# Kernel tuning notes

Measured on AMD Instinct MI355X. Metric: run time of the kernel, lower is better.

Reference implementation:

```python
import jax, jax.numpy as jnp
import numpy as np

NA, NF, EA, EF, NG = 200000, 50000, 800000, 200000, 4096
D = 128
BN_EPS = 1e-5

def _bn(x, g, b):
    m = x.mean(axis=0)
    v = x.var(axis=0)
    return g * (x - m) * jax.lax.rsqrt(v + BN_EPS) + b

def _gine(x, src, dst, edge_emb, W1, b1, g1, be1, W2, b2):
    # message = relu(x_src + edge_emb); scatter-add to dst; (1+eps)*x with eps=0
    msg = jax.nn.relu(x[src] + edge_emb)
    agg = jax.ops.segment_sum(msg, dst, num_segments=x.shape[0])
    h = x + agg
    h = jax.nn.relu(_bn(h @ W1 + b1, g1, be1))
    return h @ W2 + b2

def _seg_mean(x, idx, n):
    s = jax.ops.segment_sum(x, idx, num_segments=n)
    c = jax.ops.segment_sum(jnp.ones((x.shape[0],), x.dtype), idx, num_segments=n)
    return s / jnp.maximum(c, 1.0)[:, None]

def setup_inputs() -> dict:
    key = jax.random.key(0)
    ks = jax.random.split(key, 40)
    def nrm(i, shape, scale=0.05):
        return (jax.random.normal(ks[i], shape, dtype=jnp.float32) * scale)
    inp = {
        'atom_x': jax.random.normal(ks[0], (NA, 101), dtype=jnp.float32),
        'fg_x': jax.random.normal(ks[1], (NF, 73), dtype=jnp.float32),
        'atom_edge_attr': jax.random.normal(ks[2], (EA, 11), dtype=jnp.float32),
        'fg_edge_attr': jax.random.normal(ks[3], (EF, 101), dtype=jnp.float32),
        'atom_emb_W': nrm(4, (101, D)), 'atom_emb_b': jnp.zeros((D,), jnp.float32),
        'fg_emb_W': nrm(5, (73, D)), 'fg_emb_b': jnp.zeros((D,), jnp.float32),
        'bond_W': nrm(6, (3, 11, D)), 'bond_b': jnp.zeros((3, D), jnp.float32),
        'ag_W1': nrm(7, (3, D, 2 * D)), 'ag_b1': jnp.zeros((3, 2 * D), jnp.float32),
        'ag_g1': jnp.ones((3, 2 * D), jnp.float32), 'ag_be1': jnp.zeros((3, 2 * D), jnp.float32),
        'ag_W2': nrm(8, (3, 2 * D, D)), 'ag_b2': jnp.zeros((3, D), jnp.float32),
        'abn_g': jnp.ones((3, D), jnp.float32), 'abn_b': jnp.zeros((3, D), jnp.float32),
        'fge_W': nrm(9, (2, 101, D)), 'fge_b': jnp.zeros((2, D), jnp.float32),
        'fg_W1': nrm(10, (2, D, 2 * D)), 'fg_b1': jnp.zeros((2, 2 * D), jnp.float32),
        'fg_g1': jnp.ones((2, 2 * D), jnp.float32), 'fg_be1': jnp.zeros((2, 2 * D), jnp.float32),
        'fg_W2': nrm(11, (2, 2 * D, D)), 'fg_b2': jnp.zeros((2, D), jnp.float32),
        'fbn_g': jnp.ones((2, D), jnp.float32), 'fbn_b': jnp.zeros((2, D), jnp.float32),
        'a2f_W': nrm(12, (D, D)), 'a2f_b': jnp.zeros((D,), jnp.float32),
        'atom_edge_index': jax.random.randint(ks[13], (2, EA), 0, NA, dtype=jnp.int32),
        'fg_edge_index': jax.random.randint(ks[14], (2, EF), 0, NF, dtype=jnp.int32),
        'atom_idx': jax.random.randint(ks[15], (NA,), 0, NA, dtype=jnp.int32),
        'fg_idx': jax.random.randint(ks[16], (NA,), 0, NF, dtype=jnp.int32),
        'fg_batch': jnp.sort(jax.random.randint(ks[17], (NF,), 0, NG, dtype=jnp.int32)),
    }
    return inp

def reference(atom_x, fg_x, atom_edge_attr, fg_edge_attr, atom_emb_W, atom_emb_b, fg_emb_W, fg_emb_b, bond_W, bond_b, ag_W1, ag_b1, ag_g1, ag_be1, ag_W2, ag_b2, abn_g, abn_b, fge_W, fge_b, fg_W1, fg_b1, fg_g1, fg_be1, fg_W2, fg_b2, fbn_g, fbn_b, a2f_W, a2f_b, atom_edge_index, fg_edge_index, atom_idx, fg_idx, fg_batch):
    asrc, adst = atom_edge_index[0], atom_edge_index[1]
    fsrc, fdst = fg_edge_index[0], fg_edge_index[1]
    h = atom_x @ atom_emb_W + atom_emb_b
    for i in range(3):
        eemb = atom_edge_attr @ bond_W[i] + bond_b[i]
        h = _gine(h, asrc, adst, eemb, ag_W1[i], ag_b1[i], ag_g1[i], ag_be1[i], ag_W2[i], ag_b2[i])
        h = _bn(h, abn_g[i], abn_b[i])
        if i != 2:
            h = jax.nn.relu(h)
    a2f = _seg_mean(h[atom_idx], fg_idx, NF) @ a2f_W + a2f_b
    g = fg_x @ fg_emb_W + fg_emb_b + a2f
    for i in range(2):
        eemb = fg_edge_attr @ fge_W[i] + fge_b[i]
        g = _gine(g, fsrc, fdst, eemb, fg_W1[i], fg_b1[i], fg_g1[i], fg_be1[i], fg_W2[i], fg_b2[i])
        g = _bn(g, fbn_g[i], fbn_b[i])
        if i != 1:
            g = jax.nn.relu(g)
    return _seg_mean(g, fg_batch, NG)
```

## Files before the change

### kernel.cpp

```cpp
#include <hip/hip_runtime.h>
#include <cstddef>
#include <cstdint>

#define NA_C 200000
#define NF_C 50000
#define EA_C 800000
#define EF_C 200000
#define NG_C 4096
#define DD 128
#define HH 256
#define SC_CHUNK 2048
#define NPW 16

typedef unsigned short u16;
typedef unsigned int   u32;
typedef float f32x4 __attribute__((ext_vector_type(4)));
typedef short s16x8 __attribute__((ext_vector_type(8)));

__device__ inline float bf2f(u16 h) { return __uint_as_float(((u32)h) << 16); }
__device__ inline u16 f2bf(float f) {
    u32 u = __float_as_uint(f);
    return (u16)((u + 0x7fffu + ((u >> 16) & 1u)) >> 16);
}
__device__ inline float2 up2(u32 u) {
    return make_float2(__uint_as_float(u << 16), __uint_as_float(u & 0xffff0000u));
}
__device__ inline u32 pk2(float x, float y) { return (u32)f2bf(x) | ((u32)f2bf(y) << 16); }

__device__ inline void gll16(const void* g, void* l) {
    __builtin_amdgcn_global_load_lds(
        (const __attribute__((address_space(1))) void*)g,
        (__attribute__((address_space(3))) void*)l, 16, 0, 0);
}

__global__ __launch_bounds__(256) void gemm_b(
    const u16* __restrict__ A, const u16* __restrict__ Bt,
    const float* __restrict__ bias,
    const float* __restrict__ isum, const float* __restrict__ isq,
    const float* __restrict__ ig, const float* __restrict__ ibe, float iminv,
    const u16* __restrict__ Cadd, u16* __restrict__ C,
    int M, int K, int Ntot,
    float* __restrict__ ssum, float* __restrict__ ssq)
{
    __shared__ u16 As[4 * 128 * 8];
    __shared__ u16 Bs[4 * 128 * 8];
    __shared__ float ls[128], lq[128];
    __shared__ float sIsc[256], sIsh[256];
    const int tid  = threadIdx.x;
    const int wave = tid >> 6, lane = tid & 63;
    const int quad = lane >> 4, l15 = lane & 15;
    const int wm = (wave & 1) * 64, wn = (wave >> 1) * 64;
    const int m0 = blockIdx.y * 128, n0 = blockIdx.x * 128;
    const int r     = tid >> 1;
    const int cpair = (tid & 1) * 2;

    if (isum) {
        if (tid < K) {
            float mu = isum[tid] * iminv;
            float va = fmaxf(isq[tid] * iminv - mu * mu, 0.f);
            float s  = ig[tid] * rsqrtf(va + 1e-5f);
            sIsc[tid] = s;
            sIsh[tid] = fmaf(-mu, s, ibe[tid]);
        }
        __syncthreads();
    }

    f32x4 acc[4][4];
#pragma unroll
    for (int i = 0; i < 4; ++i)
#pragma unroll
        for (int j = 0; j < 4; ++j) acc[i][j] = (f32x4)0.f;

    const int m = m0 + r;
    for (int k0 = 0; k0 < K; k0 += 32) {
        if (isum) {
#pragma unroll
            for (int j = 0; j < 2; ++j) {
                const int cg = cpair + j;
                uint4 av = make_uint4(0, 0, 0, 0);
                if (m < M) av = *(const uint4*)(A + (size_t)m * K + k0 + cg * 8);
                u32* w = (u32*)&av;
#pragma unroll
                for (int q2 = 0; q2 < 4; ++q2) {
                    int kk = k0 + cg * 8 + q2 * 2;
                    float2 f = up2(w[q2]);
                    f.x = fmaxf(fmaf(f.x, sIsc[kk],     sIsh[kk]),     0.f);
                    f.y = fmaxf(fmaf(f.y, sIsc[kk + 1], sIsh[kk + 1]), 0.f);
                    w[q2] = pk2(f.x, f.y);
                }
                *(uint4*)&As[(cg * 128 + r) * 8] = av;
            }
        } else {
#pragma unroll
            for (int j = 0; j < 2; ++j) {
                gll16(A + (size_t)(m0 + j * 64 + lane) * K + k0 + wave * 8,
                      &As[(wave * 128 + j * 64) * 8]);
            }
        }
#pragma unroll
        for (int j = 0; j < 2; ++j) {
            gll16(Bt + (size_t)(n0 + j * 64 + lane) * K + k0 + wave * 8,
                  &Bs[(wave * 128 + j * 64) * 8]);
        }
        __syncthreads();

        s16x8 a[4], b[4];
#pragma unroll
        for (int mi = 0; mi < 4; ++mi)
            a[mi] = *(const s16x8*)&As[(quad * 128 + wm + mi * 16 + l15) * 8];
#pragma unroll
        for (int ni = 0; ni < 4; ++ni)
            b[ni] = *(const s16x8*)&Bs[(quad * 128 + wn + ni * 16 + l15) * 8];
#pragma unroll
        for (int mi = 0; mi < 4; ++mi)
#pragma unroll
            for (int ni = 0; ni < 4; ++ni)
                acc[mi][ni] = __builtin_amdgcn_mfma_f32_16x16x32_bf16(
                    a[mi], b[ni], acc[mi][ni], 0, 0, 0);
        __syncthreads();
    }

    if (ssum) {
        if (tid < 128) { ls[tid] = 0.f; lq[tid] = 0.f; }
        __syncthreads();
    }

    float cs[4] = {0.f, 0.f, 0.f, 0.f}, cq[4] = {0.f, 0.f, 0.f, 0.f};
#pragma unroll
    for (int mi = 0; mi < 4; ++mi) {
        int rowb = m0 + wm + mi * 16 + quad * 4;
#pragma unroll
        for (int ni = 0; ni < 4; ++ni) {
            int col = n0 + wn + ni * 16 + l15;
            float bv = bias[col];
#pragma unroll
            for (int rr = 0; rr < 4; ++rr) {
                int row = rowb + rr;
                if (row < M) {
                    float v = acc[mi][ni][rr] + bv;
                    size_t idx = (size_t)row * Ntot + col;
                    if (Cadd) v += bf2f(Cadd[idx]);
                    C[idx] = f2bf(v);
                    cs[ni] += v;
                    cq[ni] = fmaf(v, v, cq[ni]);
                }
            }
        }
    }

    if (ssum) {
#pragma unroll
        for (int ni = 0; ni < 4; ++ni) {
            int lc = wn + ni * 16 + l15;
            atomicAdd(&ls[lc], cs[ni]);
            atomicAdd(&lq[lc], cq[ni]);
        }
        __syncthreads();
        if (tid < 128) {
            atomicAdd(&ssum[n0 + tid], ls[tid]);
            atomicAdd(&ssq[n0 + tid], lq[tid]);
        }
    }
}

static inline void gemm_launch(hipStream_t s, const u16* A, const u16* Bt,
    const float* bias,
    const float* isum, const float* isq, const float* ig, const float* ibe,
    float iminv, const u16* Cadd, u16* C, int M, int K, int Ntot,
    float* ssum = nullptr, float* ssq = nullptr)
{
    dim3 grid(Ntot / 128, (M + 127) / 128);
    gemm_b<<<grid, dim3(256), 0, s>>>(A, Bt, bias, isum, isq, ig, ibe, iminv,
                                      Cadd, C, M, K, Ntot, ssum, ssq);
}

__global__ void cvt_pad(const float* __restrict__ src, u32* __restrict__ dst,
                        int M, int K, int Kp2)
{
    int idx = blockIdx.x * 256 + threadIdx.x;
    if (idx >= M * Kp2) return;
    int row = idx / Kp2, c = (idx - row * Kp2) * 2;
    float a = (c < K)     ? src[(size_t)row * K + c]     : 0.f;
    float b = (c + 1 < K) ? src[(size_t)row * K + c + 1] : 0.f;
    dst[idx] = pk2(a, b);
}

__global__ void cvt_pad_perm(const float* __restrict__ src, const int2* __restrict__ csr2,
                             u32* __restrict__ dst, int M, int K, int Kp2)
{
    int idx = blockIdx.x * 256 + threadIdx.x;
    if (idx >= M * Kp2) return;
    int row = idx / Kp2, c = (idx - row * Kp2) * 2;
    int srow = csr2[row].x;
    float a = (c < K)     ? src[(size_t)srow * K + c]     : 0.f;
    float b = (c + 1 < K) ? src[(size_t)srow * K + c + 1] : 0.f;
    dst[idx] = pk2(a, b);
}

__global__ void perm_attr12_k(const float* __restrict__ attr, const int2* __restrict__ csr2,
                              float* __restrict__ out, int ne)
{
    int idx = blockIdx.x * 256 + threadIdx.x;
    if (idx >= ne * 12) return;
    int e = idx / 12, k = idx - e * 12;
    int eid = csr2[e].x;
    out[idx] = (k < 11) ? attr[(size_t)eid * 11 + k] : 0.f;
}

#define NJOBS 15
struct WtJobs {
    const float* W[NJOBS];
    u16* Wt[NJOBS];
    int K[NJOBS], N[NJOBS], Kp[NJOBS], end[NJOBS];
};

__global__ void prep_wt_all(WtJobs jobs, int total)
{
    int idx = blockIdx.x * 256 + threadIdx.x;
    if (idx >= total) return;
    int j = 0;
    while (idx >= jobs.end[j]) ++j;
    int base = j ? jobs.end[j - 1] : 0;
    int loc = idx - base;
    int Kp = jobs.Kp[j];
    int n = loc / Kp, k = loc - n * Kp;
    jobs.Wt[j][loc] = (k < jobs.K[j])
        ? f2bf(jobs.W[j][(size_t)k * jobs.N[j] + n]) : (u16)0;
}

__global__ void hist_k(const int* __restrict__ idx, int n, int* __restrict__ deg)
{
    int i = blockIdx.x * 256 + threadIdx.x;
    if (i < n) atomicAdd(&deg[idx[i]], 1);
}

__global__ __launch_bounds__(256) void scan_part_k(const int* __restrict__ deg, int n,
                                                   int* __restrict__ bsum)
{
    __shared__ int ts[256];
    const int t = threadIdx.x;
    const int base = blockIdx.x * SC_CHUNK + t * 8;
    int s = 0;
#pragma unroll
    for (int j = 0; j < 8; ++j) { int i = base + j; if (i < n) s += deg[i]; }
    ts[t] = s;
    __syncthreads();
    for (int off = 128; off > 0; off >>= 1) {
        if (t < off) ts[t] += ts[t + off];
        __syncthreads();
    }
    if (t == 0) bsum[blockIdx.x] = ts[0];
}

__global__ __launch_bounds__(256) void scan_top_k(int* __restrict__ bsum, int nb)
{
    __shared__ int ss[256];
    const int t = threadIdx.x;
    int v = (t < nb) ? bsum[t] : 0;
    ss[t] = v;
    __syncthreads();
    for (int off = 1; off < 256; off <<= 1) {
        int u = (t >= off) ? ss[t - off] : 0;
        __syncthreads();
        ss[t] += u;
        __syncthreads();
    }
    if (t < nb) bsum[t] = ss[t] - v;
}

__global__ __launch_bounds__(256) void scan_emit_k(int* __restrict__ deg, int n,
                                                   const int* __restrict__ bsum,
                                                   int* __restrict__ rowptr)
{
    __shared__ int ts[256];
    const int t = threadIdx.x;
    const int base = blockIdx.x * SC_CHUNK + t * 8;
    int d[8], loc[8], s = 0;
#pragma unroll
    for (int j = 0; j < 8; ++j) {
        int i = base + j;
        d[j] = (i < n) ? deg[i] : 0;
        loc[j] = s;
        s += d[j];
    }
    ts[t] = s;
    __syncthreads();
    for (int off = 1; off < 256; off <<= 1) {
        int u = (t >= off) ? ts[t - off] : 0;
        __syncthreads();
        ts[t] += u;
        __syncthreads();
    }
    const int off0 = bsum[blockIdx.x] + (ts[t] - s);
#pragma unroll
    for (int j = 0; j < 8; ++j) {
        int i = base + j;
        if (i < n) {
            int st = off0 + loc[j];
            rowptr[i] = st;
            deg[i] = st;
            if (i == n - 1) rowptr[n] = st + d[j];
        }
    }
}

static void csr_prefix(hipStream_t s, const int* idx, int ne, int nbkt,
                       int* rowptr, int* cursor, int* bsum)
{
    hipMemsetAsync(cursor, 0, (size_t)nbkt * 4, s);
    hist_k<<<(ne + 255) / 256, 256, 0, s>>>(idx, ne, cursor);
    int nblk = (nbkt + SC_CHUNK - 1) / SC_CHUNK;
    scan_part_k<<<nblk, 256, 0, s>>>(cursor, nbkt, bsum);
    scan_top_k<<<1, 256, 0, s>>>(bsum, nblk);
    scan_emit_k<<<nblk, 256, 0, s>>>(cursor, nbkt, bsum, rowptr);
}

__global__ void fill2_k(const int* __restrict__ idx, const int* __restrict__ src,
                        int n, int* __restrict__ cursor, int2* __restrict__ csr2)
{
    int i = blockIdx.x * 256 + threadIdx.x;
    if (i < n) {
        int p = atomicAdd(&cursor[idx[i]], 1);
        csr2[p] = make_int2(i, src[i]);
    }
}

__global__ void fillm_k(const int* __restrict__ idx, const int* __restrict__ map,
                        int n, int* __restrict__ cursor, int* __restrict__ csr)
{
    int i = blockIdx.x * 256 + threadIdx.x;
    if (i < n) {
        int p = atomicAdd(&cursor[idx[i]], 1);
        csr[p] = map ? map[i] : i;
    }
}

__device__ inline void bn_lane(const float* bsum, const float* bsq,
                               const float* bg, const float* bbe, float minv,
                               int lane, float& sc0, float& sc1, float& sh0, float& sh1)
{
    float mu0 = bsum[2 * lane] * minv,     mu1 = bsum[2 * lane + 1] * minv;
    float va0 = fmaxf(bsq[2 * lane] * minv - mu0 * mu0, 0.f);
    float va1 = fmaxf(bsq[2 * lane + 1] * minv - mu1 * mu1, 0.f);
    sc0 = bg[2 * lane] * rsqrtf(va0 + 1e-5f);
    sc1 = bg[2 * lane + 1] * rsqrtf(va1 + 1e-5f);
    sh0 = fmaf(-mu0, sc0, bbe[2 * lane]);
    sh1 = fmaf(-mu1, sc1, bbe[2 * lane + 1]);
}

__global__ __launch_bounds__(256) void gine_agg_atom_b(
    const u32* __restrict__ x2, const float4* __restrict__ attrp,
    const int2* __restrict__ csr2, const int* __restrict__ rowptr,
    const float* __restrict__ Wm, const float* __restrict__ bm,
    const float* __restrict__ bsum, const float* __restrict__ bsq,
    const float* __restrict__ bg, const float* __restrict__ bbe,
    float bminv, int trelu,
    u32* __restrict__ out2, int n)
{
    const int lane = threadIdx.x & 63;
    const int v0 = (blockIdx.x * 4 + (threadIdx.x >> 6)) * NPW;
    if (v0 >= n) return;
    const int vend = (v0 + NPW < n) ? v0 + NPW : n;

    const float2 w0 = *(const float2*)&Wm[0 * 128 + 2 * lane];
    const float2 w1 = *(const float2*)&Wm[1 * 128 + 2 * lane];
    const float2 w2 = *(const float2*)&Wm[2 * 128 + 2 * lane];
    const float2 w3 = *(const float2*)&Wm[3 * 128 + 2 * lane];
    const float2 w4 = *(const float2*)&Wm[4 * 128 + 2 * lane];
    const float2 w5 = *(const float2*)&Wm[5 * 128 + 2 * lane];
    const float2 w6 = *(const float2*)&Wm[6 * 128 + 2 * lane];
    const float2 w7 = *(const float2*)&Wm[7 * 128 + 2 * lane];
    const float2 w8 = *(const float2*)&Wm[8 * 128 + 2 * lane];
    const float2 w9 = *(const float2*)&Wm[9 * 128 + 2 * lane];
    const float2 wa = *(const float2*)&Wm[10 * 128 + 2 * lane];
    const float2 bb = *(const float2*)&bm[2 * lane];

    float sc0 = 1.f, sc1 = 1.f, sh0 = 0.f, sh1 = 0.f;
    if (bsum) bn_lane(bsum, bsq, bg, bbe, bminv, lane, sc0, sc1, sh0, sh1);

    const int E0 = rowptr[v0], E1 = rowptr[vend];
    int v  = v0;
    int nb = rowptr[v0 + 1];
    u32 xs_n = (v0 + 1 < vend) ? x2[(size_t)(v0 + 1) * 64 + lane] : 0u;
    float2 acc = up2(x2[(size_t)v0 * 64 + lane]);
    acc.x = fmaf(acc.x, sc0, sh0); acc.y = fmaf(acc.y, sc1, sh1);
    if (trelu) { acc.x = fmaxf(acc.x, 0.f); acc.y = fmaxf(acc.y, 0.f); }

    if (E0 < E1) {
        int2 pc = csr2[E0];
        int2 pn = csr2[(E0 + 1 < E1) ? E0 + 1 : E0];
        float4 a0c = attrp[3 * (size_t)E0];
        float4 a1c = attrp[3 * (size_t)E0 + 1];
        float4 a2c = attrp[3 * (size_t)E0 + 2];
        u32 xc = x2[(size_t)pc.y * 64 + lane];
        for (int e = E0; e < E1; ++e) {
            const int en  = (e + 1 < E1) ? e + 1 : e;
            const int en2 = (e + 2 < E1) ? e + 2 : en;
            int2 p2 = csr2[en2];
            u32 xn = x2[(size_t)pn.y * 64 + lane];
            float4 a0n = attrp[3 * (size_t)en];
            float4 a1n = attrp[3 * (size_t)en + 1];
            float4 a2n = attrp[3 * (size_t)en + 2];
            while (e >= nb) {
                out2[(size_t)v * 64 + lane] = pk2(acc.x, acc.y);
                ++v;
                float2 nx = up2(xs_n);
                nx.x = fmaf(nx.x, sc0, sh0); nx.y = fmaf(nx.y, sc1, sh1);
                if (trelu) { nx.x = fmaxf(nx.x, 0.f); nx.y = fmaxf(nx.y, 0.f); }
                acc = nx;
                xs_n = (v + 1 < vend) ? x2[(size_t)(v + 1) * 64 + lane] : xs_n;
                nb = rowptr[v + 1];
            }
            float m0 = bb.x, m1 = bb.y;
            m0 = fmaf(a0c.x, w0.x, m0); m1 = fmaf(a0c.x, w0.y, m1);
            m0 = fmaf(a0c.y, w1.x, m0); m1 = fmaf(a0c.y, w1.y, m1);
            m0 = fmaf(a0c.z, w2.x, m0); m1 = fmaf(a0c.z, w2.y, m1);
            m0 = fmaf(a0c.w, w3.x, m0); m1 = fmaf(a0c.w, w3.y, m1);
            m0 = fmaf(a1c.x, w4.x, m0); m1 = fmaf(a1c.x, w4.y, m1);
            m0 = fmaf(a1c.y, w5.x, m0); m1 = fmaf(a1c.y, w5.y, m1);
            m0 = fmaf(a1c.z, w6.x, m0); m1 = fmaf(a1c.z, w6.y, m1);
            m0 = fmaf(a1c.w, w7.x, m0); m1 = fmaf(a1c.w, w7.y, m1);
            m0 = fmaf(a2c.x, w8.x, m0); m1 = fmaf(a2c.x, w8.y, m1);
            m0 = fmaf(a2c.y, w9.x, m0); m1 = fmaf(a2c.y, w9.y, m1);
            m0 = fmaf(a2c.z, wa.x, m0); m1 = fmaf(a2c.z, wa.y, m1);
            float2 s = up2(xc);
            s.x = fmaf(s.x, sc0, sh0); s.y = fmaf(s.y, sc1, sh1);
            if (trelu) { s.x = fmaxf(s.x, 0.f); s.y = fmaxf(s.y, 0.f); }
            acc.x += fmaxf(s.x + m0, 0.f);
            acc.y += fmaxf(s.y + m1, 0.f);
            pn = p2; xc = xn;
            a0c = a0n; a1c = a1n; a2c = a2n;
        }
    }
    for (;;) {
        out2[(size_t)v * 64 + lane] = pk2(acc.x, acc.y);
        ++v;
        if (v >= vend) break;
        float2 nx = up2(xs_n);
        nx.x = fmaf(nx.x, sc0, sh0); nx.y = fmaf(nx.y, sc1, sh1);
        if (trelu) { nx.x = fmaxf(nx.x, 0.f); nx.y = fmaxf(nx.y, 0.f); }
        acc = nx;
        xs_n = (v + 1 < vend) ? x2[(size_t)(v + 1) * 64 + lane] : xs_n;
    }
}

__global__ __launch_bounds__(256) void gine_agg_pre_b(
    const u32* __restrict__ x2, const u32* __restrict__ eemb2,
    const int2* __restrict__ csr2, const int* __restrict__ rowptr,
    const float* __restrict__ bsum, const float* __restrict__ bsq,
    const float* __restrict__ bg, const float* __restrict__ bbe,
    float bminv, int trelu,
    u32* __restrict__ out2, int n)
{
    const int lane = threadIdx.x & 63;
    const int v0 = (blockIdx.x * 4 + (threadIdx.x >> 6)) * NPW;
    if (v0 >= n) return;
    const int vend = (v0 + NPW < n) ? v0 + NPW : n;

    float sc0 = 1.f, sc1 = 1.f, sh0 = 0.f, sh1 = 0.f;
    if (bsum) bn_lane(bsum, bsq, bg, bbe, bminv, lane, sc0, sc1, sh0, sh1);

    const int E0 = rowptr[v0], E1 = rowptr[vend];
    int v  = v0;
    int nb = rowptr[v0 + 1];
    u32 xs_n = (v0 + 1 < vend) ? x2[(size_t)(v0 + 1) * 64 + lane] : 0u;
    float2 acc = up2(x2[(size_t)v0 * 64 + lane]);
    acc.x = fmaf(acc.x, sc0, sh0); acc.y = fmaf(acc.y, sc1, sh1);
    if (trelu) { acc.x = fmaxf(acc.x, 0.f); acc.y = fmaxf(acc.y, 0.f); }

    if (E0 < E1) {
        int2 pc = csr2[E0];
        int2 pn = csr2[(E0 + 1 < E1) ? E0 + 1 : E0];
        u32 xc = x2[(size_t)pc.y * 64 + lane];
        u32 mc = eemb2[(size_t)E0 * 64 + lane];
        for (int e = E0; e < E1; ++e) {
            const int en  = (e + 1 < E1) ? e + 1 : e;
            const int en2 = (e + 2 < E1) ? e + 2 : en;
            int2 p2 = csr2[en2];
            u32 xn = x2[(size_t)pn.y * 64 + lane];
            u32 mn = eemb2[(size_t)en * 64 + lane];
            while (e >= nb) {
                out2[(size_t)v * 64 + lane] = pk2(acc.x, acc.y);
                ++v;
                float2 nx = up2(xs_n);
                nx.x = fmaf(nx.x, sc0, sh0); nx.y = fmaf(nx.y, sc1, sh1);
                if (trelu) { nx.x = fmaxf(nx.x, 0.f); nx.y = fmaxf(nx.y, 0.f); }
                acc = nx;
                xs_n = (v + 1 < vend) ? x2[(size_t)(v + 1) * 64 + lane] : xs_n;
                nb = rowptr[v + 1];
            }
            float2 m = up2(mc);
            float2 s = up2(xc);
            s.x = fmaf(s.x, sc0, sh0); s.y = fmaf(s.y, sc1, sh1);
            if (trelu) { s.x = fmaxf(s.x, 0.f); s.y = fmaxf(s.y, 0.f); }
            acc.x += fmaxf(m.x + s.x, 0.f);
            acc.y += fmaxf(m.y + s.y, 0.f);
            pn = p2; xc = xn; mc = mn;
        }
    }
    for (;;) {
        out2[(size_t)v * 64 + lane] = pk2(acc.x, acc.y);
        ++v;
        if (v >= vend) break;
        float2 nx = up2(xs_n);
        nx.x = fmaf(nx.x, sc0, sh0); nx.y = fmaf(nx.y, sc1, sh1);
        if (trelu) { nx.x = fmaxf(nx.x, 0.f); nx.y = fmaxf(nx.y, 0.f); }
        acc = nx;
        xs_n = (v + 1 < vend) ? x2[(size_t)(v + 1) * 64 + lane] : xs_n;
    }
}

__global__ __launch_bounds__(256) void seg_mean_b2b(
    const u32* __restrict__ x2, const int* __restrict__ csr,
    const int* __restrict__ rowptr,
    const float* __restrict__ bsum, const float* __restrict__ bsq,
    const float* __restrict__ bg, const float* __restrict__ bbe, float bminv,
    u32* __restrict__ out2, int n)
{
    const int lane = threadIdx.x & 63;
    const int v = blockIdx.x * 4 + (threadIdx.x >> 6);
    if (v >= n) return;
    const int e0 = rowptr[v], e1 = rowptr[v + 1];
    float2 acc = make_float2(0.f, 0.f);
    if (e0 < e1) {
        int cc = csr[e0];
        int cn = csr[(e0 + 1 < e1) ? e0 + 1 : e0];
        u32 xc = x2[(size_t)cc * 64 + lane];
        for (int e = e0; e < e1; ++e) {
            const int en  = (e + 1 < e1) ? e + 1 : e;
            const int en2 = (e + 2 < e1) ? e + 2 : en;
            int c2 = csr[en2];
            u32 xn = x2[(size_t)cn * 64 + lane];
            float2 s = up2(xc);
            acc.x += s.x; acc.y += s.y;
            cn = c2; xc = xn;
        }
    }
    float inv = 1.f / fmaxf((float)(e1 - e0), 1.f);
    float2 r = make_float2(acc.x * inv, acc.y * inv);
    if (bsum) {
        if (e1 > e0) {
            float sc0, sc1, sh0, sh1;
            bn_lane(bsum, bsq, bg, bbe, bminv, lane, sc0, sc1, sh0, sh1);
            r.x = fmaf(r.x, sc0, sh0);
            r.y = fmaf(r.y, sc1, sh1);
        } else {
            r.x = 0.f; r.y = 0.f;
        }
    }
    out2[(size_t)v * 64 + lane] = pk2(r.x, r.y);
}

__global__ __launch_bounds__(256) void seg_mean_b2f(
    const u32* __restrict__ x2, const int* __restrict__ csr,
    const int* __restrict__ rowptr,
    const float* __restrict__ bsum, const float* __restrict__ bsq,
    const float* __restrict__ bg, const float* __restrict__ bbe, float bminv,
    float* __restrict__ out, int n)
{
    const int lane = threadIdx.x & 63;
    const int v = blockIdx.x * 4 + (threadIdx.x >> 6);
    if (v >= n) return;
    const int e0 = rowptr[v], e1 = rowptr[v + 1];
    float2 acc = make_float2(0.f, 0.f);
    if (e0 < e1) {
        int cc = csr[e0];
        int cn = csr[(e0 + 1 < e1) ? e0 + 1 : e0];
        u32 xc = x2[(size_t)cc * 64 + lane];
        for (int e = e0; e < e1; ++e) {
            const int en  = (e + 1 < e1) ? e + 1 : e;
            const int en2 = (e + 2 < e1) ? e + 2 : en;
            int c2 = csr[en2];
            u32 xn = x2[(size_t)cn * 64 + lane];
            float2 s = up2(xc);
            acc.x += s.x; acc.y += s.y;
            cn = c2; xc = xn;
        }
    }
    float inv = 1.f / fmaxf((float)(e1 - e0), 1.f);
    float2 r = make_float2(acc.x * inv, acc.y * inv);
    if (bsum) {
        if (e1 > e0) {
            float sc0, sc1, sh0, sh1;
            bn_lane(bsum, bsq, bg, bbe, bminv, lane, sc0, sc1, sh0, sh1);
            r.x = fmaf(r.x, sc0, sh0);
            r.y = fmaf(r.y, sc1, sh1);
        } else {
            r.x = 0.f; r.y = 0.f;
        }
    }
    *(float2*)&out[(size_t)v * 128 + lane * 2] = r;
}

extern "C" void kernel_launch(void* const* d_in, const int* in_sizes, int n_in,
                              void* d_out, int out_size, void* d_ws, size_t ws_size,
                              hipStream_t stream)
{
    const float* atom_x        = (const float*)d_in[0];
    const float* fg_x          = (const float*)d_in[1];
    const float* atom_edge_attr= (const float*)d_in[2];
    const float* fg_edge_attr  = (const float*)d_in[3];
    const float* atom_emb_W    = (const float*)d_in[4];
    const float* atom_emb_b    = (const float*)d_in[5];
    const float* fg_emb_W      = (const float*)d_in[6];
    const float* fg_emb_b      = (const float*)d_in[7];
    const float* bond_W        = (const float*)d_in[8];
    const float* bond_b        = (const float*)d_in[9];
    const float* ag_W1         = (const float*)d_in[10];
    const float* ag_b1         = (const float*)d_in[11];
    const float* ag_g1         = (const float*)d_in[12];
    const float* ag_be1        = (const float*)d_in[13];
    const float* ag_W2         = (const float*)d_in[14];
    const float* ag_b2         = (const float*)d_in[15];
    const float* abn_g         = (const float*)d_in[16];
    const float* abn_b         = (const float*)d_in[17];
    const float* fge_W         = (const float*)d_in[18];
    const float* fge_b         = (const float*)d_in[19];
    const float* fg_W1         = (const float*)d_in[20];
    const float* fg_b1         = (const float*)d_in[21];
    const float* fg_g1         = (const float*)d_in[22];
    const float* fg_be1        = (const float*)d_in[23];
    const float* fg_W2         = (const float*)d_in[24];
    const float* fg_b2         = (const float*)d_in[25];
    const float* fbn_g         = (const float*)d_in[26];
    const float* fbn_b         = (const float*)d_in[27];
    const float* a2f_W         = (const float*)d_in[28];
    const float* a2f_b         = (const float*)d_in[29];
    const int*   aei           = (const int*)d_in[30];
    const int*   fei           = (const int*)d_in[31];
    const int*   atom_idx      = (const int*)d_in[32];
    const int*   fg_idx        = (const int*)d_in[33];
    const int*   fg_batch      = (const int*)d_in[34];
    const int *asrc = aei, *adst = aei + EA_C;
    const int *fsrc = fei, *fdst = fei + EF_C;

    char* base = (char*)d_ws;
    const size_t SZ_H = (size_t)NA_C * DD * 2;
    u16* hA = (u16*)base;
    u16* hB = (u16*)(base + SZ_H);
    u16* TB = (u16*)(base + 2 * SZ_H);
    u16* XB = (u16*)(base + 2 * SZ_H + (size_t)NA_C * HH * 2);
    char* csrb = (char*)XB + SZ_H;
    int*  aR  = (int*)csrb;
    int*  aCu = aR + (NA_C + 2);
    int*  bS  = aCu + NA_C;
    int2* aE2 = (int2*)(bS + 258);
    char* wtb = (char*)(aE2 + EA_C);
    wtb = (char*)(((uintptr_t)wtb + 15) & ~(uintptr_t)15);
    u16* WT_aemb = (u16*)wtb;                 wtb += 128 * 128 * 2;
    u16* WT_aW1  = (u16*)wtb;                 wtb += 3 * 256 * 128 * 2;
    u16* WT_aW2  = (u16*)wtb;                 wtb += 3 * 128 * 256 * 2;
    u16* WT_a2f  = (u16*)wtb;                 wtb += 128 * 128 * 2;
    u16* WT_femb = (u16*)wtb;                 wtb += 128 * 96 * 2;
    u16* WT_fge  = (u16*)wtb;                 wtb += 2 * 128 * 128 * 2;
    u16* WT_fW1  = (u16*)wtb;                 wtb += 2 * 256 * 128 * 2;
    u16* WT_fW2  = (u16*)wtb;                 wtb += 2 * 128 * 256 * 2;
    float* stats = (float*)wtb;               wtb += 5120 * sizeof(float);
    float* S_SUM = stats;
    float* S_SQ  = stats + 2560;

    {
        WtJobs jb;
        int t = 0, acc = 0;
        auto add = [&](const float* W, u16* Wt, int K, int N, int Kp) {
            jb.W[t] = W; jb.Wt[t] = Wt; jb.K[t] = K; jb.N[t] = N; jb.Kp[t] = Kp;
            acc += N * Kp; jb.end[t] = acc; ++t;
        };
        add(atom_emb_W, WT_aemb, 101, 128, 128);
        add(a2f_W,      WT_a2f,  128, 128, 128);
        for (int i = 0; i < 3; ++i)
            add(ag_W1 + (size_t)i * 128 * 256, WT_aW1 + (size_t)i * 256 * 128, 128, 256, 128);
        for (int i = 0; i < 3; ++i)
            add(ag_W2 + (size_t)i * 256 * 128, WT_aW2 + (size_t)i * 128 * 256, 256, 128, 256);
        add(fg_emb_W,   WT_femb, 73, 128, 96);
        for (int i = 0; i < 2; ++i)
            add(fge_W + (size_t)i * 101 * 128, WT_fge + (size_t)i * 128 * 128, 101, 128, 128);
        for (int i = 0; i < 2; ++i)
            add(fg_W1 + (size_t)i * 128 * 256, WT_fW1 + (size_t)i * 256 * 128, 128, 256, 128);
        for (int i = 0; i < 2; ++i)
            add(fg_W2 + (size_t)i * 256 * 128, WT_fW2 + (size_t)i * 128 * 256, 256, 128, 256);
        prep_wt_all<<<(acc + 255) / 256, 256, 0, stream>>>(jb, acc);
    }
    hipMemsetAsync(stats, 0, 5120 * sizeof(float), stream);

    csr_prefix(stream, adst, EA_C, NA_C, aR, aCu, bS);
    fill2_k<<<(EA_C + 255) / 256, 256, 0, stream>>>(adst, asrc, EA_C, aCu, aE2);

    cvt_pad<<<((size_t)NA_C * 64 + 255) / 256, 256, 0, stream>>>(atom_x, (u32*)XB, NA_C, 101, 64);

    gemm_launch(stream, XB, WT_aemb, atom_emb_b,
                nullptr, nullptr, nullptr, nullptr, 0.f, nullptr, hA, NA_C, 128, 128);

    float* attrP = (float*)XB;
    perm_attr12_k<<<((size_t)EA_C * 12 + 255) / 256, 256, 0, stream>>>(
        atom_edge_attr, aE2, attrP, EA_C);

    const int agrid = (NA_C + 4 * NPW - 1) / (4 * NPW);
    u16* hc = hA;
    const float* cb_sum = nullptr; const float* cb_sq = nullptr;
    const float* cb_g = nullptr;   const float* cb_be = nullptr;
    int cur_relu = 0;
    for (int i = 0; i < 3; ++i) {
        u16* hn = (hc == hA) ? hB : hA;
        const int st1 = 2 * i, st2 = 2 * i + 1;
        gine_agg_atom_b<<<agrid, 256, 0, stream>>>(
            (const u32*)hc, (const float4*)attrP, aE2, aR,
            bond_W + (size_t)i * 11 * DD, bond_b + i * DD,
            cb_sum, cb_sq, cb_g, cb_be, 1.f / NA_C, cur_relu, (u32*)hn, NA_C);
        gemm_launch(stream, hn, WT_aW1 + (size_t)i * 256 * 128,
                    ag_b1 + i * HH, nullptr, nullptr, nullptr, nullptr, 0.f,
                    nullptr, TB, NA_C, 128, HH,
                    S_SUM + st1 * 256, S_SQ + st1 * 256);
        gemm_launch(stream, TB, WT_aW2 + (size_t)i * 128 * 256,
                    ag_b2 + i * DD,
                    S_SUM + st1 * 256, S_SQ + st1 * 256,
                    ag_g1 + i * HH, ag_be1 + i * HH, 1.f / NA_C,
                    nullptr, hn, NA_C, 256, 128,
                    S_SUM + st2 * 256, S_SQ + st2 * 256);
        cb_sum = S_SUM + st2 * 256; cb_sq = S_SQ + st2 * 256;
        cb_g = abn_g + i * DD; cb_be = abn_b + i * DD;
        cur_relu = (i != 2);
        hc = hn;
    }

    {
        int* xE = (int*)aE2;
        csr_prefix(stream, fg_idx, NA_C, NF_C, aR, aCu, bS);
        fillm_k<<<(NA_C + 255) / 256, 256, 0, stream>>>(fg_idx, atom_idx, NA_C, aCu, xE);
        seg_mean_b2b<<<(NF_C + 3) / 4, 256, 0, stream>>>(
            (const u32*)hc, xE, aR, cb_sum, cb_sq, cb_g, cb_be, 1.f / NA_C,
            (u32*)hA, NF_C);
    }
    u16* means   = hA;
    u16* a2f_lin = hA + (size_t)NF_C * DD;
    gemm_launch(stream, means, WT_a2f, a2f_b,
                nullptr, nullptr, nullptr, nullptr, 0.f, nullptr, a2f_lin, NF_C, 128, 128);

    u16* fgx_bf = hA + (size_t)NF_C * DD * 2;
    cvt_pad<<<((size_t)NF_C * 48 + 255) / 256, 256, 0, stream>>>(fg_x, (u32*)fgx_bf, NF_C, 73, 48);
    u16* g = hB;
    gemm_launch(stream, fgx_bf, WT_femb, fg_emb_b,
                nullptr, nullptr, nullptr, nullptr, 0.f, a2f_lin, g, NF_C, 96, 128);

    csr_prefix(stream, fdst, EF_C, NF_C, aR, aCu, bS);
    fill2_k<<<(EF_C + 255) / 256, 256, 0, stream>>>(fdst, fsrc, EF_C, aCu, aE2);
    cvt_pad_perm<<<((size_t)EF_C * 64 + 255) / 256, 256, 0, stream>>>(
        fg_edge_attr, aE2, (u32*)XB, EF_C, 101, 64);

    const int fgrid = (NF_C + 4 * NPW - 1) / (4 * NPW);
    u16* eemb = TB;
    u16* gn   = hA + (size_t)NF_C * DD * 2 + (size_t)NF_C * 96;
    u16* gt   = TB + (size_t)EF_C * DD;
    const float* gb_sum = nullptr; const float* gb_sq = nullptr;
    const float* gb_g = nullptr;   const float* gb_be = nullptr;
    int grelu = 0;
    for (int i = 0; i < 2; ++i) {
        const int st1 = 6 + 2 * i, st2 = 7 + 2 * i;
        gemm_launch(stream, XB, WT_fge + (size_t)i * 128 * 128,
                    fge_b + i * DD, nullptr, nullptr, nullptr, nullptr, 0.f,
                    nullptr, eemb, EF_C, 128, 128);
        gine_agg_pre_b<<<fgrid, 256, 0, stream>>>(
            (const u32*)g, (const u32*)eemb, aE2, aR,
            gb_sum, gb_sq, gb_g, gb_be, 1.f / NF_C, grelu, (u32*)gn, NF_C);
        gemm_launch(stream, gn, WT_fW1 + (size_t)i * 256 * 128,
                    fg_b1 + i * HH, nullptr, nullptr, nullptr, nullptr, 0.f,
                    nullptr, gt, NF_C, 128, HH,
                    S_SUM + st1 * 256, S_SQ + st1 * 256);
        gemm_launch(stream, gt, WT_fW2 + (size_t)i * 128 * 256,
                    fg_b2 + i * DD,
                    S_SUM + st1 * 256, S_SQ + st1 * 256,
                    fg_g1 + i * HH, fg_be1 + i * HH, 1.f / NF_C,
                    nullptr, g, NF_C, 256, 128,
                    S_SUM + st2 * 256, S_SQ + st2 * 256);
        gb_sum = S_SUM + st2 * 256; gb_sq = S_SQ + st2 * 256;
        gb_g = fbn_g + i * DD; gb_be = fbn_b + i * DD;
        grelu = (i != 1);
    }

    {
        int* bR  = (int*)(gt + (size_t)NF_C * HH);
        int* bCu = bR + (NG_C + 1);
        int* bE  = bCu + NG_C;
        csr_prefix(stream, fg_batch, NF_C, NG_C, bR, bCu, bS);
        fillm_k<<<(NF_C + 255) / 256, 256, 0, stream>>>(fg_batch, nullptr, NF_C, bCu, bE);
        seg_mean_b2f<<<(NG_C + 3) / 4, 256, 0, stream>>>(
            (const u32*)g, bE, bR, gb_sum, gb_sq, gb_g, gb_be, 1.f / NF_C,
            (float*)d_out, NG_C);
    }
}
```

Measured before the change: 2.165 ms.

## Double GEMM K-step to 64 and halve nodes per wave in aggregation

After: 2.107 ms. -2.7%, faster.

```diff
diff --git a/kernel.cpp b/kernel.cpp
--- a/kernel.cpp
+++ b/kernel.cpp
@@ -10,7 +10,7 @@
 #define DD 128
 #define HH 256
 #define SC_CHUNK 2048
-#define NPW 16
+#define NPW 8
 
 typedef unsigned short u16;
 typedef unsigned int   u32;
@@ -42,8 +42,8 @@
     int M, int K, int Ntot,
     float* __restrict__ ssum, float* __restrict__ ssq)
 {
-    __shared__ u16 As[4 * 128 * 8];
-    __shared__ u16 Bs[4 * 128 * 8];
+    __shared__ u16 As[8 * 128 * 8];
+    __shared__ u16 Bs[8 * 128 * 8];
     __shared__ float ls[128], lq[128];
     __shared__ float sIsc[256], sIsh[256];
     const int tid  = threadIdx.x;
@@ -51,8 +51,8 @@
     const int quad = lane >> 4, l15 = lane & 15;
     const int wm = (wave & 1) * 64, wn = (wave >> 1) * 64;
     const int m0 = blockIdx.y * 128, n0 = blockIdx.x * 128;
-    const int r     = tid >> 1;
-    const int cpair = (tid & 1) * 2;
+    const int r  = tid >> 1;
+    const int g0 = (tid & 1) * 4;
 
     if (isum) {
         if (tid < K) {
@@ -72,11 +72,11 @@
         for (int j = 0; j < 4; ++j) acc[i][j] = (f32x4)0.f;
 
     const int m = m0 + r;
-    for (int k0 = 0; k0 < K; k0 += 32) {
+    for (int k0 = 0; k0 < K; k0 += 64) {
         if (isum) {
 #pragma unroll
-            for (int j = 0; j < 2; ++j) {
-                const int cg = cpair + j;
+            for (int j = 0; j < 4; ++j) {
+                const int cg = g0 + j;
                 uint4 av = make_uint4(0, 0, 0, 0);
                 if (m < M) av = *(const uint4*)(A + (size_t)m * K + k0 + cg * 8);
                 u32* w = (u32*)&av;
@@ -92,31 +92,36 @@
             }
         } else {
 #pragma unroll
-            for (int j = 0; j < 2; ++j) {
-                gll16(A + (size_t)(m0 + j * 64 + lane) * K + k0 + wave * 8,
-                      &As[(wave * 128 + j * 64) * 8]);
-            }
-        }
-#pragma unroll
-        for (int j = 0; j < 2; ++j) {
-            gll16(Bt + (size_t)(n0 + j * 64 + lane) * K + k0 + wave * 8,
-                  &Bs[(wave * 128 + j * 64) * 8]);
-        }
-        __syncthreads();
-
-        s16x8 a[4], b[4];
-#pragma unroll
-        for (int mi = 0; mi < 4; ++mi)
-            a[mi] = *(const s16x8*)&As[(quad * 128 + wm + mi * 16 + l15) * 8];
-#pragma unroll
-        for (int ni = 0; ni < 4; ++ni)
-            b[ni] = *(const s16x8*)&Bs[(quad * 128 + wn + ni * 16 + l15) * 8];
-#pragma unroll
-        for (int mi = 0; mi < 4; ++mi)
+            for (int kk = 0; kk < 2; ++kk)
+#pragma unroll
+                for (int j = 0; j < 2; ++j)
+                    gll16(A + (size_t)(m0 + j * 64 + lane) * K + k0 + (wave + kk * 4) * 8,
+                          &As[((wave + kk * 4) * 128 + j * 64) * 8]);
+        }
+#pragma unroll
+        for (int kk = 0; kk < 2; ++kk)
+#pragma unroll
+            for (int j = 0; j < 2; ++j)
+                gll16(Bt + (size_t)(n0 + j * 64 + lane) * K + k0 + (wave + kk * 4) * 8,
+                      &Bs[((wave + kk * 4) * 128 + j * 64) * 8]);
+        __syncthreads();
+
+#pragma unroll
+        for (int kk = 0; kk < 2; ++kk) {
+            s16x8 a[4], b[4];
+#pragma unroll
+            for (int mi = 0; mi < 4; ++mi)
+                a[mi] = *(const s16x8*)&As[((quad + kk * 4) * 128 + wm + mi * 16 + l15) * 8];
 #pragma unroll
             for (int ni = 0; ni < 4; ++ni)
-                acc[mi][ni] = __builtin_amdgcn_mfma_f32_16x16x32_bf16(
-                    a[mi], b[ni], acc[mi][ni], 0, 0, 0);
+                b[ni] = *(const s16x8*)&Bs[((quad + kk * 4) * 128 + wn + ni * 16 + l15) * 8];
+#pragma unroll
+            for (int mi = 0; mi < 4; ++mi)
+#pragma unroll
+                for (int ni = 0; ni < 4; ++ni)
+                    acc[mi][ni] = __builtin_amdgcn_mfma_f32_16x16x32_bf16(
+                        a[mi], b[ni], acc[mi][ni], 0, 0, 0);
+        }
         __syncthreads();
     }
 
@@ -651,7 +656,7 @@
     u16* WT_aW1  = (u16*)wtb;                 wtb += 3 * 256 * 128 * 2;
     u16* WT_aW2  = (u16*)wtb;                 wtb += 3 * 128 * 256 * 2;
     u16* WT_a2f  = (u16*)wtb;                 wtb += 128 * 128 * 2;
-    u16* WT_femb = (u16*)wtb;                 wtb += 128 * 96 * 2;
+    u16* WT_femb = (u16*)wtb;                 wtb += 128 * 128 * 2;
     u16* WT_fge  = (u16*)wtb;                 wtb += 2 * 128 * 128 * 2;
     u16* WT_fW1  = (u16*)wtb;                 wtb += 2 * 256 * 128 * 2;
     u16* WT_fW2  = (u16*)wtb;                 wtb += 2 * 128 * 256 * 2;
@@ -672,7 +677,7 @@
             add(ag_W1 + (size_t)i * 128 * 256, WT_aW1 + (size_t)i * 256 * 128, 128, 256, 128);
         for (int i = 0; i < 3; ++i)
             add(ag_W2 + (size_t)i * 256 * 128, WT_aW2 + (size_t)i * 128 * 256, 256, 128, 256);
-        add(fg_emb_W,   WT_femb, 73, 128, 96);
+        add(fg_emb_W,   WT_femb, 73, 128, 128);
         for (int i = 0; i < 2; ++i)
             add(fge_W + (size_t)i * 101 * 128, WT_fge + (size_t)i * 128 * 128, 101, 128, 128);
         for (int i = 0; i < 2; ++i)
@@ -736,11 +741,11 @@
     gemm_launch(stream, means, WT_a2f, a2f_b,
                 nullptr, nullptr, nullptr, nullptr, 0.f, nullptr, a2f_lin, NF_C, 128, 128);
 
-    u16* fgx_bf = hA + (size_t)NF_C * DD * 2;
-    cvt_pad<<<((size_t)NF_C * 48 + 255) / 256, 256, 0, stream>>>(fg_x, (u32*)fgx_bf, NF_C, 73, 48);
+    u16* fgx_bf = hA + 2 * (size_t)NF_C * DD;
+    cvt_pad<<<((size_t)NF_C * 64 + 255) / 256, 256, 0, stream>>>(fg_x, (u32*)fgx_bf, NF_C, 73, 64);
     u16* g = hB;
     gemm_launch(stream, fgx_bf, WT_femb, fg_emb_b,
-                nullptr, nullptr, nullptr, nullptr, 0.f, a2f_lin, g, NF_C, 96, 128);
+                nullptr, nullptr, nullptr, nullptr, 0.f, a2f_lin, g, NF_C, 128, 128);
 
     csr_prefix(stream, fdst, EF_C, NF_C, aR, aCu, bS);
     fill2_k<<<(EF_C + 255) / 256, 256, 0, stream>>>(fdst, fsrc, EF_C, aCu, aE2);
@@ -749,7 +754,7 @@
 
     const int fgrid = (NF_C + 4 * NPW - 1) / (4 * NPW);
     u16* eemb = TB;
-    u16* gn   = hA + (size_t)NF_C * DD * 2 + (size_t)NF_C * 96;
+    u16* gn   = hA + 3 * (size_t)NF_C * DD;
     u16* gt   = TB + (size_t)EF_C * DD;
     const float* gb_sum = nullptr; const float* gb_sq = nullptr;
     const float* gb_g = nullptr;   const float* gb_be = nullptr;
```
